# Kernel tuning notes

Measured on AMD Instinct MI355X. Metric: run time of the kernel, lower is better.

Reference implementation:

```python
import jax, jax.numpy as jnp
import numpy as np
from jax import lax

T = 8192; BLK = 32; M = 64; C = 32; D = 512; HH = 256; L = 6; TEMP = 1.0

def _gru(x, Wih, Whh, bih, bhh, reverse=False):
    # x: (S, B, in) -> (S, B, h); PyTorch GRU cell math
    h0 = jnp.zeros((x.shape[1], Whh.shape[0]), x.dtype)
    xs = x[::-1] if reverse else x
    gi = xs @ Wih + bih
    def step(h, g):
        gh = h @ Whh + bhh
        ir, iz, inn = jnp.split(g, 3, -1)
        hr, hz, hn = jnp.split(gh, 3, -1)
        r = jax.nn.sigmoid(ir + hr)
        z = jax.nn.sigmoid(iz + hz)
        n = jnp.tanh(inn + r * hn)
        h = (1.0 - z) * n + z * h
        return h, h
    _, hs = lax.scan(step, h0, gi)
    return hs[::-1] if reverse else hs

def _xattn(X, Y, Xpos, Ypos, Wq, Wk, Wv, Wo, bo):
    # Y queries X; single head with head_dim = D (X2Y_map)
    q = (Y + Ypos) @ Wq
    k = (X + Xpos) @ Wk
    v = X @ Wv
    logits = jnp.einsum('ybd,xbd->byx', q, k) / jnp.sqrt(jnp.float32(q.shape[-1]))
    attn = jax.nn.softmax(logits, -1)
    out = jnp.einsum('byx,xbd->ybd', attn, v) @ Wo + bo
    return out, attn, logits

def _conv1(x, W, b, dil=1):
    y = lax.conv_general_dilated(x, W, (1,), 'SAME', rhs_dilation=(dil,), dimension_numbers=('NCH', 'OIH', 'NCH'))
    return y + b[None, :, None]

def _sim(x, W, b, text):
    v = x @ W + b
    v = v / jnp.linalg.norm(v, axis=-1, keepdims=True)
    t = text / jnp.linalg.norm(text, axis=-1, keepdims=True)
    return jnp.einsum('tbh,ch->tbc', v, t) / TEMP

def _segments(frame_feature, Wf2c, bf2c, text):
    # host-side argmax -> contiguous-run segmentation (mirrors utils.parse_label on CPU)
    sim = _sim(frame_feature, Wf2c, bf2c, text)
    pred = np.asarray(jnp.argmax(sim[:, 0], -1))
    change = np.concatenate([[0], (np.diff(pred) != 0).astype(np.int64)])
    seg_id = np.cumsum(change)
    S = int(seg_id[-1]) + 1
    starts = np.concatenate([[0], np.flatnonzero(change)])
    ends = np.concatenate([starts[1:] - 1, [len(pred) - 1]])
    centers = (starts + ends) // 2
    return jnp.asarray(seg_id), S, jnp.asarray(centers)

def _core(p, seg_id, S, centers):
    ff = p['frame_feature']
    cnt = jax.ops.segment_sum(jnp.ones((T,), jnp.float32), seg_id, S)
    seg = jax.ops.segment_sum(ff, seg_id, S) / cnt[:, None, None]  # frame->seg mean pool
    hf = _gru(seg, p['sg_Wih_f'], p['sg_Whh_f'], p['sg_bih_f'], p['sg_bhh_f'])
    hb = _gru(seg, p['sg_Wih_b'], p['sg_Whh_b'], p['sg_bih_b'], p['sg_bhh_b'], reverse=True)
    seg = jax.nn.relu(jnp.concatenate([hf, hb], -1)) @ p['Wcomb'] + p['bcomb']
    seg_pos = p['frame_pos'][centers]
    af, _, _ = _xattn(seg, p['action_feature'], seg_pos, p['action_pos'], p['f2a_Wq'], p['f2a_Wk'], p['f2a_Wv'], p['f2a_Wo'], p['f2a_bo'])
    af = _gru(af, p['ag_Wih'], p['ag_Whh'], p['ag_bih'], p['ag_bhh'])  # action branch GRU
    seg2, _, _ = _xattn(af, seg, p['action_pos'], seg_pos, p['a2f_Wq'], p['a2f_Wk'], p['a2f_Wv'], p['a2f_Wo'], p['a2f_bo'])
    s2f = seg2[seg_id]  # seg->frame upsample
    ff2 = jax.nn.relu(jnp.concatenate([s2f, ff], -1) @ p['Wsf'] + p['bsf'])
    x = jnp.transpose(ff2[:, 0])[None]  # (1, D, T)
    x = _conv1(x, p['tcn_in_W'], p['tcn_in_b'])
    for i in range(L):  # dilated residual TCN (MSTCN)
        y = jax.nn.relu(_conv1(x, p['tcn_dW'][i], p['tcn_db'][i], dil=2 ** i))
        x = x + _conv1(y, p['tcn_pW'][i], p['tcn_pb'][i])
    x = _conv1(x, p['tcn_out_W'], p['tcn_out_b'])
    ff_out = jnp.transpose(x[0])[:, None, :]
    return ff_out, af, seg2

def setup_inputs():
    ks = iter(jax.random.split(jax.random.key(0), 80))
    def rn(*shape):
        return jax.random.normal(next(ks), shape, dtype=jnp.float32)
    def z(n):
        return jnp.zeros((n,), jnp.float32)
    s = 0.05
    base = rn(T // BLK, 1, D)
    frame_feature = jnp.repeat(base, BLK, axis=0) + 0.01 * rn(T, 1, D)
    return {
        'frame_feature': frame_feature,
        'action_feature': rn(M, 1, D),
        'frame_pos': 0.02 * rn(T, 1, D),
        'action_pos': 0.02 * rn(M, 1, D),
        'text_emb': rn(C, 512),
        'Wf2c': s * rn(D, 512), 'bf2c': z(512),
        'Wa2c': s * rn(D, 512), 'ba2c': z(512),
        'Ws2c': s * rn(D, 512), 'bs2c': z(512),
        'sg_Wih_f': s * rn(D, 3 * HH), 'sg_Whh_f': s * rn(HH, 3 * HH), 'sg_bih_f': z(3 * HH), 'sg_bhh_f': z(3 * HH),
        'sg_Wih_b': s * rn(D, 3 * HH), 'sg_Whh_b': s * rn(HH, 3 * HH), 'sg_bih_b': z(3 * HH), 'sg_bhh_b': z(3 * HH),
        'Wcomb': s * rn(D, D), 'bcomb': z(D),
        'f2a_Wq': s * rn(D, D), 'f2a_Wk': s * rn(D, D), 'f2a_Wv': s * rn(D, D), 'f2a_Wo': s * rn(D, D), 'f2a_bo': z(D),
        'ag_Wih': s * rn(D, 3 * D), 'ag_Whh': s * rn(D, 3 * D), 'ag_bih': z(3 * D), 'ag_bhh': z(3 * D),
        'a2f_Wq': s * rn(D, D), 'a2f_Wk': s * rn(D, D), 'a2f_Wv': s * rn(D, D), 'a2f_Wo': s * rn(D, D), 'a2f_bo': z(D),
        'Wsf': s * rn(2 * D, D), 'bsf': z(D),
        'tcn_in_W': s * rn(D, D, 1), 'tcn_in_b': z(D),
        'tcn_dW': s * rn(L, D, D, 3), 'tcn_db': jnp.zeros((L, D), jnp.float32),
        'tcn_pW': s * rn(L, D, D, 1), 'tcn_pb': jnp.zeros((L, D), jnp.float32),
        'tcn_out_W': s * rn(D, D, 1), 'tcn_out_b': z(D),
    }

def reference(frame_feature, action_feature, frame_pos, action_pos, text_emb, Wf2c, bf2c, Wa2c, ba2c, Ws2c, bs2c, sg_Wih_f, sg_Whh_f, sg_bih_f, sg_bhh_f, sg_Wih_b, sg_Whh_b, sg_bih_b, sg_bhh_b, Wcomb, bcomb, f2a_Wq, f2a_Wk, f2a_Wv, f2a_Wo, f2a_bo, ag_Wih, ag_Whh, ag_bih, ag_bhh, a2f_Wq, a2f_Wk, a2f_Wv, a2f_Wo, a2f_bo, Wsf, bsf, tcn_in_W, tcn_in_b, tcn_dW, tcn_db, tcn_pW, tcn_pb, tcn_out_W, tcn_out_b):
    p = dict(locals())
    seg_id, S, centers = _segments(frame_feature, Wf2c, bf2c, text_emb)
    ff_out, af, seg2 = _core(p, seg_id, S, centers)
    frame_sim = _sim(ff_out, Wf2c, bf2c, text_emb)
    action_sim = _sim(af, Wa2c, ba2c, text_emb)
    seg_sim = _sim(seg2, Ws2c, bs2c, text_emb)
    return ff_out, af, frame_sim, action_sim, seg_sim
```

## Files before the change

### kernel.cpp

```cpp
#include <hip/hip_runtime.h>
#include <cstdint>
#include <cstddef>

__device__ __forceinline__ float sigf(float x) { return 1.f / (1.f + expf(-x)); }

__device__ __forceinline__ unsigned packh(float a, float b) {
  union { unsigned u; _Float16 h[2]; } cv;
  cv.h[0] = (_Float16)a; cv.h[1] = (_Float16)b; return cv.u;
}
__device__ __forceinline__ float2 uph(unsigned u) {
  union { unsigned uu; _Float16 h[2]; } cv; cv.uu = u;
  return make_float2((float)cv.h[0], (float)cv.h[1]);
}

typedef _Float16 f16x8 __attribute__((ext_vector_type(8)));
typedef float f32x16 __attribute__((ext_vector_type(16)));

static constexpr int TT = 8192;
static constexpr int MM = 64;
static constexpr int CC = 32;
static constexpr int DD = 512;
static constexpr unsigned GUARD_MAX = 1u << 30;
static constexpr unsigned HSENT = 0x7FC07FC0u;

__global__ void nanfill_k(float* __restrict__ p, long n) {
  long i = (long)blockIdx.x * 256 + threadIdx.x;
  long stride = (long)gridDim.x * 256;
  const float qnan = __int_as_float(0x7fc00000);
  for (; i < n; i += stride) p[i] = qnan;
}
__global__ void sfill_k(unsigned* __restrict__ p, long n) {
  long i = (long)blockIdx.x * 256 + threadIdx.x;
  long stride = (long)gridDim.x * 256;
  for (; i < n; i += stride) p[i] = HSENT;
}

__global__ void copy_k(const float* __restrict__ a, float* __restrict__ o, int n) {
  int i = blockIdx.x * 256 + threadIdx.x;
  if (i < n) o[i] = a[i];
}
__global__ void addff_k(const float* __restrict__ a, const float* __restrict__ b, float* __restrict__ o, int n) {
  int i = blockIdx.x * 256 + threadIdx.x;
  if (i < n) o[i] = a[i] + b[i];
}
__global__ void acomb_k(const unsigned* __restrict__ hf, const unsigned* __restrict__ hb,
                        float* __restrict__ o, int n) {
  int i = blockIdx.x * 256 + threadIdx.x;
  if (i >= n) return;
  int s = i >> 9, j = i & 511;
  const unsigned pk = (j < 256) ? hf[(size_t)s * 128 + (j >> 1)]
                                : hb[(size_t)s * 128 + ((j - 256) >> 1)];
  const float2 two = uph(pk);
  const float v = (j & 1) ? two.y : two.x;
  o[i] = fmaxf(v, 0.f);
}
__global__ void gatherpos_k(const float* __restrict__ fpos, const int* __restrict__ centers,
                            float* __restrict__ segpos, int n) {
  int i = blockIdx.x * 256 + threadIdx.x;
  if (i >= n) return;
  int s = i >> 9, dd = i & 511;
  int ct = centers[s];
  ct = ct < 0 ? 0 : (ct > TT - 1 ? TT - 1 : ct);
  segpos[i] = fpos[(size_t)ct * 512 + dd];
}

__global__ void tnorm_k(const float* __restrict__ text, float* __restrict__ tnorm) {
  int c = blockIdx.x * 256 + threadIdx.x;
  if (c >= 32) return;
  float s = 0.f;
  for (int dd = 0; dd < 512; dd++) { float v = text[(size_t)c * 512 + dd]; s += v * v; }
  tnorm[c] = sqrtf(s);
}

__global__ void prepM_k(const float* __restrict__ W, const float* __restrict__ b,
                        const float* __restrict__ text, const float* __restrict__ tnorm,
                        float* __restrict__ M, float* __restrict__ bdot) {
  int idx = blockIdx.x * 256 + threadIdx.x;
  if (idx < 512 * 32) {
    int k = idx >> 5, c = idx & 31;
    const float* wr = W + (size_t)k * 512;
    const float* tr = text + (size_t)c * 512;
    float s = 0.f;
    for (int dd = 0; dd < 512; dd++) s += wr[dd] * tr[dd];
    M[idx] = s / tnorm[c];
  }
  if (idx < 32) {
    const float* tr = text + (size_t)idx * 512;
    float s = 0.f;
    for (int dd = 0; dd < 512; dd++) s += b[dd] * tr[dd];
    bdot[idx] = s / tnorm[idx];
  }
}

__launch_bounds__(256)
__global__ void fargmax_k(const float* __restrict__ ff, const float* __restrict__ M,
                          const float* __restrict__ bdot, int* __restrict__ pred) {
  const int r = blockIdx.x * 8 + (threadIdx.x >> 5);
  const int c = threadIdx.x & 31;
  const float* fr = ff + (size_t)r * 512;
  float acc = bdot[c];
  for (int k = 0; k < 512; k++) acc += fr[k] * M[k * 32 + c];
  float best = acc; int bidx = c;
  for (int off = 16; off >= 1; off >>= 1) {
    const float ov = __shfl_xor(best, off);
    const int oi = __shfl_xor(bidx, off);
    if (ov > best || (ov == best && oi < bidx)) { best = ov; bidx = oi; }
  }
  if (c == 0) pred[r] = bidx;
}

__global__ void nlogit_k(const float* __restrict__ Q, const float* __restrict__ Kk,
                         float* __restrict__ L, int NY, int NX) {
  int idx = blockIdx.x * 256 + threadIdx.x;
  if (idx >= NY * NX) return;
  int y = idx / NX, x = idx - y * NX;
  const float* qr = Q + (size_t)y * 512;
  const float* kr = Kk + (size_t)x * 512;
  float d = 0.f;
  for (int k = 0; k < 512; k++) d += qr[k] * kr[k];
  L[idx] = d * 0.044194173824159216f;
}
__global__ void nsoft_k(float* __restrict__ L, int NY, int NX) {
  int y = blockIdx.x * 256 + threadIdx.x;
  if (y >= NY) return;
  float* row = L + (size_t)y * NX;
  float m = row[0];
  for (int x = 1; x < NX; x++) m = fmaxf(m, row[x]);
  float s = 0.f;
  for (int x = 0; x < NX; x++) { float p = expf(row[x] - m); row[x] = p; s += p; }
  const float inv = 1.f / s;
  for (int x = 0; x < NX; x++) row[x] *= inv;
}
__global__ void nav_k(const float* __restrict__ P, const float* __restrict__ V,
                      float* __restrict__ O, int NY, int NX) {
  int idx = blockIdx.x * 256 + threadIdx.x;
  if (idx >= NY * 512) return;
  int y = idx >> 9, dd = idx & 511;
  const float* pr = P + (size_t)y * NX;
  float o = 0.f;
  for (int x = 0; x < NX; x++) o += pr[x] * V[(size_t)x * 512 + dd];
  O[idx] = o;
}

__global__ void segscan_k(const int* __restrict__ pred, int* __restrict__ segid,
                          int* __restrict__ starts, int* __restrict__ centers,
                          int* __restrict__ cnts) {
  __shared__ int base[256];
  __shared__ int SS;
  const int tid = threadIdx.x;
  int lc = 0;
  unsigned flags = 0;
  int prev = (tid > 0) ? pred[tid * 32 - 1] : 0;
  for (int i = 0; i < 32; i++) {
    const int t = tid * 32 + i;
    const int cur = pred[t];
    const int c = (t > 0) && (cur != prev);
    prev = cur;
    flags |= ((unsigned)c) << i;
    lc += c;
  }
  base[tid] = lc;
  __syncthreads();
  if (tid == 0) {
    int run = 0;
    for (int i = 0; i < 256; i++) { const int v = base[i]; base[i] = run; run += v; }
    SS = run + 1;
  }
  __syncthreads();
  int b = base[tid];
  for (int i = 0; i < 32; i++) {
    const int t = tid * 32 + i;
    if ((flags >> i) & 1u) { b++; starts[b] = t; }
    segid[t] = b;
  }
  if (tid == 0) starts[0] = 0;
  __threadfence_block();
  __syncthreads();
  const int S = SS;
  for (int s = tid; s < TT; s += 256) {
    if (s < S) {
      const int e = (s == S - 1) ? (TT - 1) : (starts[s + 1] - 1);
      centers[s] = (starts[s] + e) >> 1;
      cnts[s] = e - starts[s] + 1;
    } else {
      starts[s] = 0; cnts[s] = 1; centers[s] = 0;
    }
  }
}

__global__ void segmean_k(const float* __restrict__ ff, const int* __restrict__ starts,
                          const int* __restrict__ cnts, float* __restrict__ segmean, int S) {
  int idx = blockIdx.x * 256 + threadIdx.x;
  if (idx >= S * 512) return;
  int s = idx >> 9, dd = idx & 511;
  int st = starts[s], n = cnts[s];
  st = st < 0 ? 0 : (st > TT - 1 ? TT - 1 : st);
  n = n < 1 ? 1 : n;
  if (st + n > TT) n = TT - st;
  float a = 0.f;
  for (int t = st; t < st + n; t++) a += ff[(size_t)t * 512 + dd];
  segmean[idx] = a / (float)n;
}

__launch_bounds__(192)
__global__ void gru_seg_mb_k(const float* __restrict__ gi_f, const float* __restrict__ gi_b,
                             const float* __restrict__ Whh_f, const float* __restrict__ bhh_f,
                             const float* __restrict__ Whh_b, const float* __restrict__ bhh_b,
                             unsigned* __restrict__ hf, unsigned* __restrict__ hb, int S) {
  const int dir = blockIdx.x >> 2;
  const int part = blockIdx.x & 3;
  const float* gi = dir ? gi_b : gi_f;
  const float* Whh = dir ? Whh_b : Whh_f;
  const float* bhh = dir ? bhh_b : bhh_f;
  unsigned* ho = dir ? hb : hf;
  const int tid = threadIdx.x;
  const int h0 = part * 64;
  const int w0 = h0 >> 1;
  const int grp = tid >> 6;
  const int jj = tid & 63;
  const int j = grp * 256 + h0 + jj;
  __shared__ __align__(16) unsigned wlds[128 * 192];
  __shared__ __align__(16) unsigned hpk[128];
  __shared__ float rbuf[64], zbuf[64], gnbuf[64];
  for (int e = tid; e < 128 * 192; e += 192) {
    const int q = e / 768, rem = e % 768;
    const int g = rem >> 2, r = rem & 3;
    const int i2 = q * 4 + r;
    const int gg = (g >> 6) * 256 + h0 + (g & 63);
    wlds[e] = packh(Whh[(size_t)(2 * i2) * 768 + gg], Whh[(size_t)(2 * i2 + 1) * 768 + gg]);
  }
  for (int e = tid; e < 128; e += 192) hpk[e] = 0u;
  const float bj = bhh[j];
  float h_reg = 0.f;
  __syncthreads();
  const uint4* hp4 = reinterpret_cast<const uint4*>(hpk);
  const uint4* wp4 = reinterpret_cast<const uint4*>(wlds);
  int s = dir ? (S - 1) : 0;
  float g_j = gi[(size_t)s * 768 + j];
  float g_n = (tid < 64) ? gi[(size_t)s * 768 + 512 + h0 + tid] : 0.f;
  for (int step = 0; step < S; step++) {
    float a0 = 0.f, a1 = 0.f, a2 = 0.f, a3 = 0.f;
#pragma unroll 8
    for (int q = 0; q < 32; q++) {
      const uint4 h4 = hp4[q];
      const uint4 w4 = wp4[q * 192 + tid];
      const float2 hh0 = uph(h4.x), hh1 = uph(h4.y), hh2 = uph(h4.z), hh3 = uph(h4.w);
      const float2 ww0 = uph(w4.x), ww1 = uph(w4.y), ww2 = uph(w4.z), ww3 = uph(w4.w);
      a0 += hh0.x * ww0.x + hh0.y * ww0.y;
      a1 += hh1.x * ww1.x + hh1.y * ww1.y;
      a2 += hh2.x * ww2.x + hh2.y * ww2.y;
      a3 += hh3.x * ww3.x + hh3.y * ww3.y;
    }
    const float gh = bj + (a0 + a1) + (a2 + a3);
    if (grp == 0)      rbuf[jj] = sigf(g_j + gh);
    else if (grp == 1) zbuf[jj] = sigf(g_j + gh);
    else               gnbuf[jj] = gh;
    __syncthreads();
    if (tid < 64) {
      const float nval = tanhf(g_n + rbuf[tid] * gnbuf[tid]);
      const float hn = (1.f - zbuf[tid]) * nval + zbuf[tid] * h_reg;
      h_reg = hn;
      const float hnb = __shfl_down(hn, 1);
      if ((tid & 1) == 0) {
        const unsigned pk = packh(hn, hnb);
        hpk[w0 + (tid >> 1)] = pk;
        __hip_atomic_store(&ho[(size_t)s * 128 + w0 + (tid >> 1)], pk,
                           __ATOMIC_RELAXED, __HIP_MEMORY_SCOPE_AGENT);
      }
    }
    const int sn = dir ? (s - 1) : (s + 1);
    if (step + 1 < S) {
      g_j = gi[(size_t)sn * 768 + j];
      if (tid < 64) g_n = gi[(size_t)sn * 768 + 512 + h0 + tid];
    }
    __syncthreads();
    if (tid < 96) {
      const int re = (tid < w0) ? tid : tid + 32;
      unsigned v = __hip_atomic_load(&ho[(size_t)s * 128 + re],
                                     __ATOMIC_RELAXED, __HIP_MEMORY_SCOPE_AGENT);
      unsigned guard = 0;
      while (v == HSENT && ++guard < GUARD_MAX) {
        __builtin_amdgcn_s_sleep(1);
        v = __hip_atomic_load(&ho[(size_t)s * 128 + re],
                              __ATOMIC_RELAXED, __HIP_MEMORY_SCOPE_AGENT);
      }
      hpk[re] = v;
    }
    __syncthreads();
    s = sn;
  }
}

__launch_bounds__(128)
__global__ void gru_act_mb_k(const float* __restrict__ gi, const float* __restrict__ Whh,
                             const float* __restrict__ bhh, float* __restrict__ hout,
                             int steps) {
  const int part = blockIdx.x;
  const int tid = threadIdx.x;
  const int h0 = part * 32;
  const int grp = tid >> 5;
  const int jj = tid & 31;
  const bool act = (tid < 96);
  const int j = act ? (grp * 512 + h0 + jj) : 0;
  __shared__ __align__(16) unsigned wlds[256 * 96];
  __shared__ __align__(16) unsigned hpk[256];
  __shared__ float rbuf[32], zbuf[32], gnbuf[32];
  for (int e = tid; e < 256 * 96; e += 128) {
    const int q = e / 384, rem = e % 384;
    const int g = rem >> 2, r = rem & 3;
    const int i2 = q * 4 + r;
    const int gg = (g >> 5) * 512 + h0 + (g & 31);
    wlds[e] = packh(Whh[(size_t)(2 * i2) * 1536 + gg], Whh[(size_t)(2 * i2 + 1) * 1536 + gg]);
  }
  for (int e = tid; e < 256; e += 128) hpk[e] = 0u;
  const float bj = act ? bhh[j] : 0.f;
  float h_reg = 0.f;
  __syncthreads();
  const uint4* hp4 = reinterpret_cast<const uint4*>(hpk);
  const uint4* wp4 = reinterpret_cast<const uint4*>(wlds);
  float g_j = act ? gi[j] : 0.f;
  float g_n = (tid < 32) ? gi[1024 + h0 + tid] : 0.f;
  const int gown0 = h0 >> 2;
  for (int step = 0; step < steps; step++) {
    if (act) {
      float a0 = 0.f, a1 = 0.f, a2 = 0.f, a3 = 0.f;
#pragma unroll 8
      for (int q = 0; q < 64; q++) {
        const uint4 h4 = hp4[q];
        const uint4 w4 = wp4[q * 96 + tid];
        const float2 hh0 = uph(h4.x), hh1 = uph(h4.y), hh2 = uph(h4.z), hh3 = uph(h4.w);
        const float2 ww0 = uph(w4.x), ww1 = uph(w4.y), ww2 = uph(w4.z), ww3 = uph(w4.w);
        a0 += hh0.x * ww0.x + hh0.y * ww0.y;
        a1 += hh1.x * ww1.x + hh1.y * ww1.y;
        a2 += hh2.x * ww2.x + hh2.y * ww2.y;
        a3 += hh3.x * ww3.x + hh3.y * ww3.y;
      }
      const float gh = bj + (a0 + a1) + (a2 + a3);
      if (grp == 0)      rbuf[jj] = sigf(g_j + gh);
      else if (grp == 1) zbuf[jj] = sigf(g_j + gh);
      else               gnbuf[jj] = gh;
    }
    __syncthreads();
    if (tid < 32) {
      const float nval = tanhf(g_n + rbuf[tid] * gnbuf[tid]);
      const float hn = (1.f - zbuf[tid]) * nval + zbuf[tid] * h_reg;
      h_reg = hn;
      __hip_atomic_store(&hout[(size_t)step * 512 + h0 + tid], hn,
                         __ATOMIC_RELAXED, __HIP_MEMORY_SCOPE_AGENT);
      const float hnb = __shfl_down(hn, 1);
      if ((tid & 1) == 0) hpk[(h0 + tid) >> 1] = packh(hn, hnb);
    }
    if (step + 1 < steps) {
      if (act) g_j = gi[(size_t)(step + 1) * 1536 + j];
      if (tid < 32) g_n = gi[(size_t)(step + 1) * 1536 + 1024 + h0 + tid];
    }
    __syncthreads();
    {
      const int g = tid;
      if (g < gown0 || g >= gown0 + 8) {
        const float* gp = hout + (size_t)step * 512 + 4 * g;
        float x0, x1, x2, x3;
        unsigned guard = 0;
        do {
          x0 = __hip_atomic_load(gp + 0, __ATOMIC_RELAXED, __HIP_MEMORY_SCOPE_AGENT);
          x1 = __hip_atomic_load(gp + 1, __ATOMIC_RELAXED, __HIP_MEMORY_SCOPE_AGENT);
          x2 = __hip_atomic_load(gp + 2, __ATOMIC_RELAXED, __HIP_MEMORY_SCOPE_AGENT);
          x3 = __hip_atomic_load(gp + 3, __ATOMIC_RELAXED, __HIP_MEMORY_SCOPE_AGENT);
          if (x0 == x0 && x1 == x1 && x2 == x2 && x3 == x3) break;
          __builtin_amdgcn_s_sleep(1);
        } while (++guard < GUARD_MAX);
        hpk[2 * g + 0] = packh(x0, x1);
        hpk[2 * g + 1] = packh(x2, x3);
      }
    }
    __syncthreads();
  }
}

__launch_bounds__(256)
__global__ void gemmm_k(const float* __restrict__ A, const float* __restrict__ B,
                        const float* __restrict__ bias, float* __restrict__ C,
                        int M, int N, int K) {
  __shared__ __align__(16) _Float16 As16[64][72];
  __shared__ __align__(16) _Float16 Bs16[128][72];
  const int n0 = blockIdx.x * 128, m0 = blockIdx.y * 64;
  const int tid = threadIdx.x;
  const int l = tid & 63, w = tid >> 6;
  const int wm = w & 1, wn = w >> 1;
  const int l31 = l & 31, q = l >> 5;
  f32x16 acc0, acc1;
#pragma unroll
  for (int i = 0; i < 16; i++) { acc0[i] = 0.f; acc1[i] = 0.f; }
  const int am = tid >> 2, ak0 = (tid & 3) * 16;
  const int bk = tid >> 2, bn0 = (tid & 3) * 32;
  for (int kc = 0; kc < K; kc += 64) {
    __syncthreads();
#pragma unroll
    for (int kk = 0; kk < 16; kk += 4) {
      const float4 av = *reinterpret_cast<const float4*>(A + (size_t)(m0 + am) * K + kc + ak0 + kk);
      As16[am][ak0 + kk + 0] = (_Float16)av.x; As16[am][ak0 + kk + 1] = (_Float16)av.y;
      As16[am][ak0 + kk + 2] = (_Float16)av.z; As16[am][ak0 + kk + 3] = (_Float16)av.w;
    }
#pragma unroll
    for (int nn = 0; nn < 32; nn += 4) {
      const float4 bv = *reinterpret_cast<const float4*>(B + (size_t)(kc + bk) * N + n0 + bn0 + nn);
      Bs16[bn0 + nn + 0][bk] = (_Float16)bv.x; Bs16[bn0 + nn + 1][bk] = (_Float16)bv.y;
      Bs16[bn0 + nn + 2][bk] = (_Float16)bv.z; Bs16[bn0 + nn + 3][bk] = (_Float16)bv.w;
    }
    __syncthreads();
#pragma unroll
    for (int ks = 0; ks < 4; ks++) {
      const int k0 = ks * 16 + q * 8;
      const f16x8 a = *reinterpret_cast<const f16x8*>(&As16[wm * 32 + l31][k0]);
      const f16x8 b0 = *reinterpret_cast<const f16x8*>(&Bs16[wn * 64 + l31][k0]);
      acc0 = __builtin_amdgcn_mfma_f32_32x32x16_f16(a, b0, acc0, 0, 0, 0);
      const f16x8 b1 = *reinterpret_cast<const f16x8*>(&Bs16[wn * 64 + 32 + l31][k0]);
      acc1 = __builtin_amdgcn_mfma_f32_32x32x16_f16(a, b1, acc1, 0, 0, 0);
    }
  }
#pragma unroll
  for (int r = 0; r < 16; r++) {
    const int m = m0 + wm * 32 + (r & 3) + 8 * (r >> 2) + 4 * q;
    {
      const int n = n0 + wn * 64 + l31;
      float v = acc0[r];
      if (bias) v += bias[n];
      C[(size_t)m * N + n] = v;
    }
    {
      const int n = n0 + wn * 64 + 32 + l31;
      float v = acc1[r];
      if (bias) v += bias[n];
      C[(size_t)m * N + n] = v;
    }
  }
}

__launch_bounds__(256)
__global__ void ff2m_k(const float* __restrict__ seg2, const float* __restrict__ ff,
                       const int* __restrict__ segid, const float* __restrict__ Wsf,
                       const float* __restrict__ bsf, float* __restrict__ Y, int S) {
  __shared__ __align__(16) _Float16 As16[64][72];
  __shared__ __align__(16) _Float16 Bs16[128][72];
  const int t0 = blockIdx.x * 128, nd0 = blockIdx.y * 64;
  const int tid = threadIdx.x;
  const int l = tid & 63, w = tid >> 6;
  const int wm = w & 1, wn = w >> 1;
  const int l31 = l & 31, q = l >> 5;
  f32x16 acc0, acc1;
#pragma unroll
  for (int i = 0; i < 16; i++) { acc0[i] = 0.f; acc1[i] = 0.f; }
  const int ak = tid >> 2, an0 = (tid & 3) * 16;
  const int bt = tid >> 1, bk0 = (tid & 1) * 32;
  const int tglob = t0 + bt;
  int sid = segid[tglob];
  sid = sid < 0 ? 0 : (sid >= S ? S - 1 : sid);
  for (int kc = 0; kc < 1024; kc += 64) {
    __syncthreads();
#pragma unroll
    for (int nn = 0; nn < 16; nn += 4) {
      const float4 wv = *reinterpret_cast<const float4*>(Wsf + (size_t)(kc + ak) * 512 + nd0 + an0 + nn);
      As16[an0 + nn + 0][ak] = (_Float16)wv.x; As16[an0 + nn + 1][ak] = (_Float16)wv.y;
      As16[an0 + nn + 2][ak] = (_Float16)wv.z; As16[an0 + nn + 3][ak] = (_Float16)wv.w;
    }
    {
      const float* src = (kc < 512) ? (seg2 + (size_t)sid * 512 + kc + bk0)
                                    : (ff + (size_t)tglob * 512 + (kc - 512) + bk0);
#pragma unroll
      for (int kk = 0; kk < 32; kk += 4) {
        const float4 xv = *reinterpret_cast<const float4*>(src + kk);
        Bs16[bt][bk0 + kk + 0] = (_Float16)xv.x; Bs16[bt][bk0 + kk + 1] = (_Float16)xv.y;
        Bs16[bt][bk0 + kk + 2] = (_Float16)xv.z; Bs16[bt][bk0 + kk + 3] = (_Float16)xv.w;
      }
    }
    __syncthreads();
#pragma unroll
    for (int ks = 0; ks < 4; ks++) {
      const int k0 = ks * 16 + q * 8;
      const f16x8 a = *reinterpret_cast<const f16x8*>(&As16[wm * 32 + l31][k0]);
      const f16x8 b0 = *reinterpret_cast<const f16x8*>(&Bs16[wn * 64 + l31][k0]);
      acc0 = __builtin_amdgcn_mfma_f32_32x32x16_f16(a, b0, acc0, 0, 0, 0);
      const f16x8 b1 = *reinterpret_cast<const f16x8*>(&Bs16[wn * 64 + 32 + l31][k0]);
      acc1 = __builtin_amdgcn_mfma_f32_32x32x16_f16(a, b1, acc1, 0, 0, 0);
    }
  }
#pragma unroll
  for (int r = 0; r < 16; r++) {
    const int nd = nd0 + wm * 32 + (r & 3) + 8 * (r >> 2) + 4 * q;
    const float bb = bsf[nd];
    {
      const int t = t0 + wn * 64 + l31;
      Y[(size_t)nd * TT + t] = fmaxf(acc0[r] + bb, 0.f);
    }
    {
      const int t = t0 + wn * 64 + 32 + l31;
      Y[(size_t)nd * TT + t] = fmaxf(acc1[r] + bb, 0.f);
    }
  }
}

template<int NTAPS, int RELU, int RES>
__launch_bounds__(256)
__global__ void convm_k(const float* __restrict__ X, const float* __restrict__ W,
                        const float* __restrict__ bias, const float* __restrict__ Res,
                        float* __restrict__ Y, int dil) {
  const int d = (NTAPS == 3) ? dil : 0;
  const int width = 128 + 2 * d;
  __shared__ __align__(16) _Float16 Ws16[NTAPS][64][72];
  __shared__ __align__(16) _Float16 Xs16[192][72];
  const int t0 = blockIdx.x * 128, c0 = blockIdx.y * 64;
  const int tid = threadIdx.x;
  const int l = tid & 63, w = tid >> 6;
  const int wm = w & 1, wn = w >> 1;
  const int l31 = l & 31, q = l >> 5;
  f32x16 acc0, acc1;
#pragma unroll
  for (int i = 0; i < 16; i++) { acc0[i] = 0.f; acc1[i] = 0.f; }
  const int xk = tid >> 2;
  const int xu0 = tid & 3;
  for (int kc = 0; kc < 512; kc += 64) {
    __syncthreads();
    {
      const float* xr = X + (size_t)(kc + xk) * TT;
      for (int u = xu0; u < width; u += 4) {
        const int gt = t0 - d + u;
        const float v = (gt >= 0 && gt < TT) ? xr[gt] : 0.f;
        Xs16[u][xk] = (_Float16)v;
      }
    }
    if (NTAPS == 3) {
      for (int e = tid; e < 64 * 48; e += 256) {
        const int c = e / 48;
        const int f0 = (e - c * 48) * 4;
        const float4 wv = *reinterpret_cast<const float4*>(
            W + (size_t)(c0 + c) * 1536 + (size_t)kc * 3 + f0);
        const float vv[4] = {wv.x, wv.y, wv.z, wv.w};
#pragma unroll
        for (int t = 0; t < 4; t++) {
          const int f = f0 + t;
          Ws16[f % 3][c][f / 3] = (_Float16)vv[t];
        }
      }
    } else {
      for (int e = tid; e < 1024; e += 256) {
        const int c = e >> 4, i0 = (e & 15) << 2;
        const float4 wv = *reinterpret_cast<const float4*>(W + (size_t)(c0 + c) * 512 + kc + i0);
        Ws16[0][c][i0 + 0] = (_Float16)wv.x; Ws16[0][c][i0 + 1] = (_Float16)wv.y;
        Ws16[0][c][i0 + 2] = (_Float16)wv.z; Ws16[0][c][i0 + 3] = (_Float16)wv.w;
      }
    }
    __syncthreads();
#pragma unroll
    for (int tap = 0; tap < NTAPS; tap++) {
#pragma unroll
      for (int ks = 0; ks < 4; ks++) {
        const int k0 = ks * 16 + q * 8;
        const f16x8 a = *reinterpret_cast<const f16x8*>(&Ws16[tap][wm * 32 + l31][k0]);
        const int row0 = wn * 64 + l31 + tap * d;
        const f16x8 b0 = *reinterpret_cast<const f16x8*>(&Xs16[row0][k0]);
        acc0 = __builtin_amdgcn_mfma_f32_32x32x16_f16(a, b0, acc0, 0, 0, 0);
        const f16x8 b1 = *reinterpret_cast<const f16x8*>(&Xs16[row0 + 32][k0]);
        acc1 = __builtin_amdgcn_mfma_f32_32x32x16_f16(a, b1, acc1, 0, 0, 0);
      }
    }
  }
#pragma unroll
  for (int r = 0; r < 16; r++) {
    const int m = wm * 32 + (r & 3) + 8 * (r >> 2) + 4 * q;
    const int c = c0 + m;
    const float bb = bias[c];
    {
      const int t = t0 + wn * 64 + l31;
      float v = acc0[r] + bb;
      if (RES) v += Res[(size_t)c * TT + t];
      if (RELU) v = fmaxf(v, 0.f);
      Y[(size_t)c * TT + t] = v;
    }
    {
      const int t = t0 + wn * 64 + 32 + l31;
      float v = acc1[r] + bb;
      if (RES) v += Res[(size_t)c * TT + t];
      if (RELU) v = fmaxf(v, 0.f);
      Y[(size_t)c * TT + t] = v;
    }
  }
}

__launch_bounds__(256)
__global__ void temit_k(const float* __restrict__ Xin, float* __restrict__ outp,
                        float* __restrict__ Aout) {
  __shared__ float tile[32][33];
  const int t0 = blockIdx.x * 32, d0 = blockIdx.y * 32;
  const int lx = threadIdx.x & 31, ly = threadIdx.x >> 5;
#pragma unroll
  for (int r = 0; r < 4; r++)
    tile[ly + 8 * r][lx] = Xin[(size_t)(d0 + ly + 8 * r) * TT + t0 + lx];
  __syncthreads();
#pragma unroll
  for (int r = 0; r < 4; r++) {
    const int t = t0 + ly + 8 * r, dd = d0 + lx;
    const float v = tile[lx][ly + 8 * r];
    outp[(size_t)t * 512 + dd] = v;
    Aout[(size_t)t * 512 + dd] = v;
  }
}

__launch_bounds__(256)
__global__ void csim_k(const float* __restrict__ V, const float* __restrict__ text,
                       const float* __restrict__ tnorm, float* __restrict__ out) {
  __shared__ float vs[512];
  __shared__ float red[4];
  const int r = blockIdx.x, tid = threadIdx.x;
  const float a = V[(size_t)r * 512 + tid];
  const float b = V[(size_t)r * 512 + 256 + tid];
  vs[tid] = a; vs[tid + 256] = b;
  float ssp = a * a + b * b;
  for (int off = 32; off >= 1; off >>= 1) ssp += __shfl_xor(ssp, off);
  if ((tid & 63) == 0) red[tid >> 6] = ssp;
  __syncthreads();
  const float ss = red[0] + red[1] + red[2] + red[3];
  const int c = tid >> 3, p = tid & 7;
  const float* tr = text + (size_t)c * 512 + p * 64;
  const float* vr = vs + p * 64;
  float d = 0.f;
#pragma unroll
  for (int k = 0; k < 64; k++) d += vr[k] * tr[k];
  for (int off = 4; off >= 1; off >>= 1) d += __shfl_xor(d, off);
  if (p == 0) out[(size_t)r * 32 + c] = d / (sqrtf(ss) * tnorm[c]);
}

extern "C" void kernel_launch(void* const* d_in, const int* in_sizes, int n_in,
                              void* d_out, int out_size, void* d_ws, size_t ws_size,
                              hipStream_t stream) {
  const float* in_ff   = (const float*)d_in[0];
  const float* in_act  = (const float*)d_in[1];
  const float* in_fpos = (const float*)d_in[2];
  const float* in_apos = (const float*)d_in[3];
  const float* in_text = (const float*)d_in[4];
  const float* Wf2c = (const float*)d_in[5];  const float* bf2c = (const float*)d_in[6];
  const float* Wa2c = (const float*)d_in[7];  const float* ba2c = (const float*)d_in[8];
  const float* Ws2c = (const float*)d_in[9];  const float* bs2c = (const float*)d_in[10];
  const float* Wih_f = (const float*)d_in[11]; const float* Whh_f = (const float*)d_in[12];
  const float* bih_f = (const float*)d_in[13]; const float* bhh_f = (const float*)d_in[14];
  const float* Wih_b = (const float*)d_in[15]; const float* Whh_b = (const float*)d_in[16];
  const float* bih_b = (const float*)d_in[17]; const float* bhh_b = (const float*)d_in[18];
  const float* Wcomb = (const float*)d_in[19]; const float* bcomb = (const float*)d_in[20];
  const float* f2a_Wq = (const float*)d_in[21]; const float* f2a_Wk = (const float*)d_in[22];
  const float* f2a_Wv = (const float*)d_in[23]; const float* f2a_Wo = (const float*)d_in[24];
  const float* f2a_bo = (const float*)d_in[25];
  const float* ag_Wih = (const float*)d_in[26]; const float* ag_Whh = (const float*)d_in[27];
  const float* ag_bih = (const float*)d_in[28]; const float* ag_bhh = (const float*)d_in[29];
  const float* a2f_Wq = (const float*)d_in[30]; const float* a2f_Wk = (const float*)d_in[31];
  const float* a2f_Wv = (const float*)d_in[32]; const float* a2f_Wo = (const float*)d_in[33];
  const float* a2f_bo = (const float*)d_in[34];
  const float* Wsf = (const float*)d_in[35]; const float* bsf = (const float*)d_in[36];
  const float* tcn_inW = (const float*)d_in[37]; const float* tcn_inb = (const float*)d_in[38];
  const float* tcn_dW = (const float*)d_in[39]; const float* tcn_db = (const float*)d_in[40];
  const float* tcn_pW = (const float*)d_in[41]; const float* tcn_pb = (const float*)d_in[42];
  const float* tcn_outW = (const float*)d_in[43]; const float* tcn_outb = (const float*)d_in[44];

  int S = (out_size - (TT * DD + MM * DD + TT * CC + MM * CC)) / CC;
  if (S < 1) S = 1;
  if (S > TT) S = TT;
  const int Spad = (S + 63) & ~63;

  char* ws = (char*)d_ws;
  size_t off = 0;
  auto alloc = [&](size_t b) -> char* { char* p = ws + off; off += (b + 255) & ~(size_t)255; return p; };
  float* Mmat = (float*)alloc((size_t)512 * 32 * 4);
  float* bdot = (float*)alloc(32 * 4);
  const size_t BTD = (size_t)TT * DD * 4;
  float* bufA = (float*)alloc(BTD);
  float* bufB = (float*)alloc(BTD);
  int* pred    = (int*)alloc((size_t)TT * 4);
  int* segid   = (int*)alloc((size_t)TT * 4);
  int* starts  = (int*)alloc((size_t)TT * 4);
  int* centers = (int*)alloc((size_t)TT * 4);
  int* cnts    = (int*)alloc((size_t)TT * 4);
  float* tnorm = (float*)alloc(32 * 4);
  float* segmean = (float*)alloc((size_t)Spad * 512 * 4);
  float* gif  = (float*)alloc((size_t)Spad * 768 * 4);
  float* gib  = (float*)alloc((size_t)Spad * 768 * 4);
  unsigned* hfb = (unsigned*)alloc((size_t)Spad * 128 * 4);
  unsigned* hbb = (unsigned*)alloc((size_t)Spad * 128 * 4);
  float* acmb = (float*)alloc((size_t)Spad * 512 * 4);
  float* segc = (float*)alloc((size_t)Spad * 512 * 4);
  float* segpos = (float*)alloc((size_t)Spad * 512 * 4);
  float* kin  = (float*)alloc((size_t)Spad * 512 * 4);
  float* kf2a = (float*)alloc((size_t)Spad * 512 * 4);
  float* vf2a = (float*)alloc((size_t)Spad * 512 * 4);
  float* q2   = (float*)alloc((size_t)Spad * 512 * 4);
  float* att2 = (float*)alloc((size_t)Spad * 512 * 4);
  float* seg2 = (float*)alloc((size_t)Spad * 512 * 4);
  float* vseg = (float*)alloc((size_t)Spad * 512 * 4);
  float* pbuf = (float*)alloc((size_t)64 * Spad * 4);
  float* qin  = (float*)alloc((size_t)64 * 512 * 4);
  float* qf2a = (float*)alloc((size_t)64 * 512 * 4);
  float* att1 = (float*)alloc((size_t)64 * 512 * 4);
  float* af0  = (float*)alloc((size_t)64 * 512 * 4);
  float* aggi = (float*)alloc((size_t)64 * 1536 * 4);
  float* afg  = (float*)alloc((size_t)64 * 512 * 4);
  float* k2in = (float*)alloc((size_t)64 * 512 * 4);
  float* k2   = (float*)alloc((size_t)64 * 512 * 4);
  float* v2   = (float*)alloc((size_t)64 * 512 * 4);
  float* vaf  = (float*)alloc((size_t)64 * 512 * 4);
  (void)ws_size; (void)in_sizes; (void)n_in;

  float* outp = (float*)d_out;
  float* out_ff   = outp;
  float* out_af   = outp + (size_t)TT * DD;
  float* out_fsim = out_af + (size_t)MM * DD;
  float* out_asim = out_fsim + (size_t)TT * CC;
  float* out_ssim = out_asim + (size_t)MM * CC;

  auto GR = [](long n) { return (unsigned)((n + 255) / 256); };
  const unsigned Sg = (unsigned)(Spad / 64);

  tnorm_k<<<1, 256, 0, stream>>>(in_text, tnorm);

  sfill_k<<<64, 256, 0, stream>>>(hfb, (long)Spad * 128);
  sfill_k<<<64, 256, 0, stream>>>(hbb, (long)Spad * 128);
  nanfill_k<<<32, 256, 0, stream>>>(afg, (long)64 * 512);

  prepM_k<<<64, 256, 0, stream>>>(Wf2c, bf2c, in_text, tnorm, Mmat, bdot);
  fargmax_k<<<TT / 8, 256, 0, stream>>>(in_ff, Mmat, bdot, pred);
  segscan_k<<<1, 256, 0, stream>>>(pred, segid, starts, centers, cnts);
  segmean_k<<<GR((long)S * 512), 256, 0, stream>>>(in_ff, starts, cnts, segmean, S);

  gemmm_k<<<dim3(6, Sg), 256, 0, stream>>>(segmean, Wih_f, bih_f, gif, Spad, 768, 512);
  gemmm_k<<<dim3(6, Sg), 256, 0, stream>>>(segmean, Wih_b, bih_b, gib, Spad, 768, 512);
  gru_seg_mb_k<<<8, 192, 0, stream>>>(gif, gib, Whh_f, bhh_f, Whh_b, bhh_b, hfb, hbb, S);
  acomb_k<<<GR((long)S * 512), 256, 0, stream>>>(hfb, hbb, acmb, S * 512);
  gemmm_k<<<dim3(4, Sg), 256, 0, stream>>>(acmb, Wcomb, bcomb, segc, Spad, 512, 512);
  gatherpos_k<<<GR((long)S * 512), 256, 0, stream>>>(in_fpos, centers, segpos, S * 512);

  addff_k<<<GR(64 * 512), 256, 0, stream>>>(in_act, in_apos, qin, 64 * 512);
  addff_k<<<GR((long)S * 512), 256, 0, stream>>>(segc, segpos, kin, S * 512);
  gemmm_k<<<dim3(4, 1), 256, 0, stream>>>(qin, f2a_Wq, nullptr, qf2a, 64, 512, 512);
  gemmm_k<<<dim3(4, Sg), 256, 0, stream>>>(kin, f2a_Wk, nullptr, kf2a, Spad, 512, 512);
  gemmm_k<<<dim3(4, Sg), 256, 0, stream>>>(segc, f2a_Wv, nullptr, vf2a, Spad, 512, 512);
  nlogit_k<<<GR((long)64 * S), 256, 0, stream>>>(qf2a, kf2a, pbuf, 64, S);
  nsoft_k<<<1, 256, 0, stream>>>(pbuf, 64, S);
  nav_k<<<GR(64 * 512), 256, 0, stream>>>(pbuf, vf2a, att1, 64, S);
  gemmm_k<<<dim3(4, 1), 256, 0, stream>>>(att1, f2a_Wo, f2a_bo, af0, 64, 512, 512);

  gemmm_k<<<dim3(12, 1), 256, 0, stream>>>(af0, ag_Wih, ag_bih, aggi, 64, 1536, 512);
  gru_act_mb_k<<<16, 128, 0, stream>>>(aggi, ag_Whh, ag_bhh, afg, MM);
  copy_k<<<GR(64 * 512), 256, 0, stream>>>(afg, out_af, 64 * 512);

  addff_k<<<GR(64 * 512), 256, 0, stream>>>(afg, in_apos, k2in, 64 * 512);
  gemmm_k<<<dim3(4, Sg), 256, 0, stream>>>(kin, a2f_Wq, nullptr, q2, Spad, 512, 512);
  gemmm_k<<<dim3(4, 1), 256, 0, stream>>>(k2in, a2f_Wk, nullptr, k2, 64, 512, 512);
  gemmm_k<<<dim3(4, 1), 256, 0, stream>>>(afg, a2f_Wv, nullptr, v2, 64, 512, 512);
  nlogit_k<<<GR((long)S * 64), 256, 0, stream>>>(q2, k2, pbuf, S, 64);
  nsoft_k<<<GR(S), 256, 0, stream>>>(pbuf, S, 64);
  nav_k<<<GR((long)S * 512), 256, 0, stream>>>(pbuf, v2, att2, S, 64);
  gemmm_k<<<dim3(4, Sg), 256, 0, stream>>>(att2, a2f_Wo, a2f_bo, seg2, Spad, 512, 512);

  ff2m_k<<<dim3(64, 8), 256, 0, stream>>>(seg2, in_ff, segid, Wsf, bsf, bufA, S);
  convm_k<1, 0, 0><<<dim3(64, 8), 256, 0, stream>>>(bufA, tcn_inW, tcn_inb, nullptr, bufB, 1);
  for (int l = 0; l < 6; l++) {
    convm_k<3, 1, 0><<<dim3(64, 8), 256, 0, stream>>>(
        bufB, tcn_dW + (size_t)l * 512 * 512 * 3, tcn_db + (size_t)l * 512, nullptr, bufA, 1 << l);
    convm_k<1, 0, 1><<<dim3(64, 8), 256, 0, stream>>>(
        bufA, tcn_pW + (size_t)l * 512 * 512, tcn_pb + (size_t)l * 512, bufB, bufB, 1);
  }
  convm_k<1, 0, 0><<<dim3(64, 8), 256, 0, stream>>>(bufB, tcn_outW, tcn_outb, nullptr, bufA, 1);
  temit_k<<<dim3(256, 16), 256, 0, stream>>>(bufA, out_ff, bufB);

  gemmm_k<<<dim3(4, 128), 256, 0, stream>>>(bufB, Wf2c, bf2c, bufA, TT, 512, 512);
  csim_k<<<TT, 256, 0, stream>>>(bufA, in_text, tnorm, out_fsim);
  gemmm_k<<<dim3(4, 1), 256, 0, stream>>>(afg, Wa2c, ba2c, vaf, 64, 512, 512);
  csim_k<<<64, 256, 0, stream>>>(vaf, in_text, tnorm, out_asim);
  gemmm_k<<<dim3(4, Sg), 256, 0, stream>>>(seg2, Ws2c, bs2c, vseg, Spad, 512, 512);
  csim_k<<<(unsigned)S, 256, 0, stream>>>(vseg, in_text, tnorm, out_ssim);
}
```

Measured before the change: 3.761 ms.

## Move cross-attention logits and AV products to MFMA GEMMs, fuse position adds

The naive per-element logit, softmax and attention-value kernels are replaced by an MFMA-based Q·K^T kernel, a block-parallel row softmax that zero-fills padded columns, and the existing MFMA GEMM for P·V. The separate elementwise add kernels for positional embeddings are folded into the GEMM A-operand load through an optional second input. This removes scalar dot-product loops and several launches and intermediate buffers. In exchange, the logits and probabilities now pass through fp16 in the MFMA path, and correctness relies on padded rows and columns being handled by the zero-fill and the Mv guard.

```diff
diff --git a/kernel.cpp b/kernel.cpp
--- a/kernel.cpp
+++ b/kernel.cpp
@@ -38,10 +38,6 @@
 __global__ void copy_k(const float* __restrict__ a, float* __restrict__ o, int n) {
   int i = blockIdx.x * 256 + threadIdx.x;
   if (i < n) o[i] = a[i];
-}
-__global__ void addff_k(const float* __restrict__ a, const float* __restrict__ b, float* __restrict__ o, int n) {
-  int i = blockIdx.x * 256 + threadIdx.x;
-  if (i < n) o[i] = a[i] + b[i];
 }
 __global__ void acomb_k(const unsigned* __restrict__ hf, const unsigned* __restrict__ hb,
                         float* __restrict__ o, int n) {
@@ -107,39 +103,6 @@
     if (ov > best || (ov == best && oi < bidx)) { best = ov; bidx = oi; }
   }
   if (c == 0) pred[r] = bidx;
-}
-
-__global__ void nlogit_k(const float* __restrict__ Q, const float* __restrict__ Kk,
-                         float* __restrict__ L, int NY, int NX) {
-  int idx = blockIdx.x * 256 + threadIdx.x;
-  if (idx >= NY * NX) return;
-  int y = idx / NX, x = idx - y * NX;
-  const float* qr = Q + (size_t)y * 512;
-  const float* kr = Kk + (size_t)x * 512;
-  float d = 0.f;
-  for (int k = 0; k < 512; k++) d += qr[k] * kr[k];
-  L[idx] = d * 0.044194173824159216f;
-}
-__global__ void nsoft_k(float* __restrict__ L, int NY, int NX) {
-  int y = blockIdx.x * 256 + threadIdx.x;
-  if (y >= NY) return;
-  float* row = L + (size_t)y * NX;
-  float m = row[0];
-  for (int x = 1; x < NX; x++) m = fmaxf(m, row[x]);
-  float s = 0.f;
-  for (int x = 0; x < NX; x++) { float p = expf(row[x] - m); row[x] = p; s += p; }
-  const float inv = 1.f / s;
-  for (int x = 0; x < NX; x++) row[x] *= inv;
-}
-__global__ void nav_k(const float* __restrict__ P, const float* __restrict__ V,
-                      float* __restrict__ O, int NY, int NX) {
-  int idx = blockIdx.x * 256 + threadIdx.x;
-  if (idx >= NY * 512) return;
-  int y = idx >> 9, dd = idx & 511;
-  const float* pr = P + (size_t)y * NX;
-  float o = 0.f;
-  for (int x = 0; x < NX; x++) o += pr[x] * V[(size_t)x * 512 + dd];
-  O[idx] = o;
 }
 
 __global__ void segscan_k(const int* __restrict__ pred, int* __restrict__ segid,
@@ -378,7 +341,8 @@
 }
 
 __launch_bounds__(256)
-__global__ void gemmm_k(const float* __restrict__ A, const float* __restrict__ B,
+__global__ void gemmm_k(const float* __restrict__ A, const float* __restrict__ A2,
+                        const float* __restrict__ B,
                         const float* __restrict__ bias, float* __restrict__ C,
                         int M, int N, int K) {
   __shared__ __align__(16) _Float16 As16[64][72];
@@ -397,7 +361,11 @@
     __syncthreads();
 #pragma unroll
     for (int kk = 0; kk < 16; kk += 4) {
-      const float4 av = *reinterpret_cast<const float4*>(A + (size_t)(m0 + am) * K + kc + ak0 + kk);
+      float4 av = *reinterpret_cast<const float4*>(A + (size_t)(m0 + am) * K + kc + ak0 + kk);
+      if (A2) {
+        const float4 a2 = *reinterpret_cast<const float4*>(A2 + (size_t)(m0 + am) * K + kc + ak0 + kk);
+        av.x += a2.x; av.y += a2.y; av.z += a2.z; av.w += a2.w;
+      }
       As16[am][ak0 + kk + 0] = (_Float16)av.x; As16[am][ak0 + kk + 1] = (_Float16)av.y;
       As16[am][ak0 + kk + 2] = (_Float16)av.z; As16[am][ak0 + kk + 3] = (_Float16)av.w;
     }
@@ -434,6 +402,74 @@
       C[(size_t)m * N + n] = v;
     }
   }
+}
+
+__launch_bounds__(256)
+__global__ void gemmnt_k(const float* __restrict__ A, const float* __restrict__ B,
+                         float* __restrict__ C, int Mv, int Nld, int K, float scale) {
+  __shared__ __align__(16) _Float16 As16[64][72];
+  __shared__ __align__(16) _Float16 Bs16[64][72];
+  const int n0 = blockIdx.x * 64, m0 = blockIdx.y * 64;
+  const int tid = threadIdx.x;
+  const int l = tid & 63, w = tid >> 6;
+  const int wm = w & 1, wn = w >> 1;
+  const int l31 = l & 31, q = l >> 5;
+  f32x16 acc;
+#pragma unroll
+  for (int i = 0; i < 16; i++) acc[i] = 0.f;
+  const int am = tid >> 2, ak0 = (tid & 3) * 16;
+  for (int kc = 0; kc < K; kc += 64) {
+    __syncthreads();
+#pragma unroll
+    for (int kk = 0; kk < 16; kk += 4) {
+      const float4 av = *reinterpret_cast<const float4*>(A + (size_t)(m0 + am) * K + kc + ak0 + kk);
+      As16[am][ak0 + kk + 0] = (_Float16)av.x; As16[am][ak0 + kk + 1] = (_Float16)av.y;
+      As16[am][ak0 + kk + 2] = (_Float16)av.z; As16[am][ak0 + kk + 3] = (_Float16)av.w;
+      const float4 bv = *reinterpret_cast<const float4*>(B + (size_t)(n0 + am) * K + kc + ak0 + kk);
+      Bs16[am][ak0 + kk + 0] = (_Float16)bv.x; Bs16[am][ak0 + kk + 1] = (_Float16)bv.y;
+      Bs16[am][ak0 + kk + 2] = (_Float16)bv.z; Bs16[am][ak0 + kk + 3] = (_Float16)bv.w;
+    }
+    __syncthreads();
+#pragma unroll
+    for (int ks = 0; ks < 4; ks++) {
+      const int k0 = ks * 16 + q * 8;
+      const f16x8 a = *reinterpret_cast<const f16x8*>(&As16[wm * 32 + l31][k0]);
+      const f16x8 b = *reinterpret_cast<const f16x8*>(&Bs16[wn * 32 + l31][k0]);
+      acc = __builtin_amdgcn_mfma_f32_32x32x16_f16(a, b, acc, 0, 0, 0);
+    }
+  }
+#pragma unroll
+  for (int r = 0; r < 16; r++) {
+    const int m = m0 + wm * 32 + (r & 3) + 8 * (r >> 2) + 4 * q;
+    const int n = n0 + wn * 32 + l31;
+    if (m < Mv) C[(size_t)m * Nld + n] = acc[r] * scale;
+  }
+}
+
+__launch_bounds__(256)
+__global__ void psoft_k(float* __restrict__ L, int NXs, int NV) {
+  float* row = L + (size_t)blockIdx.x * NXs;
+  __shared__ float redm[4], reds[4];
+  const int tid = threadIdx.x;
+  float m = -3.4e38f;
+  for (int x = tid; x < NV; x += 256) m = fmaxf(m, row[x]);
+  for (int off = 32; off >= 1; off >>= 1) m = fmaxf(m, __shfl_xor(m, off));
+  if ((tid & 63) == 0) redm[tid >> 6] = m;
+  __syncthreads();
+  m = fmaxf(fmaxf(redm[0], redm[1]), fmaxf(redm[2], redm[3]));
+  float s = 0.f;
+  for (int x = tid; x < NV; x += 256) {
+    const float p = expf(row[x] - m);
+    row[x] = p;
+    s += p;
+  }
+  for (int off = 32; off >= 1; off >>= 1) s += __shfl_xor(s, off);
+  if ((tid & 63) == 0) reds[tid >> 6] = s;
+  __syncthreads();
+  s = reds[0] + reds[1] + reds[2] + reds[3];
+  const float inv = 1.f / s;
+  for (int x = tid; x < NV; x += 256) row[x] *= inv;
+  for (int x = NV + tid; x < NXs; x += 256) row[x] = 0.f;
 }
 
 __launch_bounds__(256)
@@ -686,7 +722,6 @@
   float* acmb = (float*)alloc((size_t)Spad * 512 * 4);
   float* segc = (float*)alloc((size_t)Spad * 512 * 4);
   float* segpos = (float*)alloc((size_t)Spad * 512 * 4);
-  float* kin  = (float*)alloc((size_t)Spad * 512 * 4);
   float* kf2a = (float*)alloc((size_t)Spad * 512 * 4);
   float* vf2a = (float*)alloc((size_t)Spad * 512 * 4);
   float* q2   = (float*)alloc((size_t)Spad * 512 * 4);
@@ -694,13 +729,11 @@
   float* seg2 = (float*)alloc((size_t)Spad * 512 * 4);
   float* vseg = (float*)alloc((size_t)Spad * 512 * 4);
   float* pbuf = (float*)alloc((size_t)64 * Spad * 4);
-  float* qin  = (float*)alloc((size_t)64 * 512 * 4);
   float* qf2a = (float*)alloc((size_t)64 * 512 * 4);
   float* att1 = (float*)alloc((size_t)64 * 512 * 4);
   float* af0  = (float*)alloc((size_t)64 * 512 * 4);
   float* aggi = (float*)alloc((size_t)64 * 1536 * 4);
   float* afg  = (float*)alloc((size_t)64 * 512 * 4);
-  float* k2in = (float*)alloc((size_t)64 * 512 * 4);
   float* k2   = (float*)alloc((size_t)64 * 512 * 4);
   float* v2   = (float*)alloc((size_t)64 * 512 * 4);
   float* vaf  = (float*)alloc((size_t)64 * 512 * 4);
@@ -715,6 +748,7 @@
 
   auto GR = [](long n) { return (unsigned)((n + 255) / 256); };
   const unsigned Sg = (unsigned)(Spad / 64);
+  const float ATTS = 0.044194173824159216f;
 
   tnorm_k<<<1, 256, 0, stream>>>(in_text, tnorm);
 
@@ -727,35 +761,32 @@
   segscan_k<<<1, 256, 0, stream>>>(pred, segid, starts, centers, cnts);
   segmean_k<<<GR((long)S * 512), 256, 0, stream>>>(in_ff, starts, cnts, segmean, S);
 
-  gemmm_k<<<dim3(6, Sg), 256, 0, stream>>>(segmean, Wih_f, bih_f, gif, Spad, 768, 512);
-  gemmm_k<<<dim3(6, Sg), 256, 0, stream>>>(segmean, Wih_b, bih_b, gib, Spad, 768, 512);
+  gemmm_k<<<dim3(6, Sg), 256, 0, stream>>>(segmean, nullptr, Wih_f, bih_f, gif, Spad, 768, 512);
+  gemmm_k<<<dim3(6, Sg), 256, 0, stream>>>(segmean, nullptr, Wih_b, bih_b, gib, Spad, 768, 512);
   gru_seg_mb_k<<<8, 192, 0, stream>>>(gif, gib, Whh_f, bhh_f, Whh_b, bhh_b, hfb, hbb, S);
   acomb_k<<<GR((long)S * 512), 256, 0, stream>>>(hfb, hbb, acmb, S * 512);
-  gemmm_k<<<dim3(4, Sg), 256, 0, stream>>>(acmb, Wcomb, bcomb, segc, Spad, 512, 512);
+  gemmm_k<<<dim3(4, Sg), 256, 0, stream>>>(acmb, nullptr, Wcomb, bcomb, segc, Spad, 512, 512);
   gatherpos_k<<<GR((long)S * 512), 256, 0, stream>>>(in_fpos, centers, segpos, S * 512);
 
-  addff_k<<<GR(64 * 512), 256, 0, stream>>>(in_act, in_apos, qin, 64 * 512);
-  addff_k<<<GR((long)S * 512), 256, 0, stream>>>(segc, segpos, kin, S * 512);
-  gemmm_k<<<dim3(4, 1), 256, 0, stream>>>(qin, f2a_Wq, nullptr, qf2a, 64, 512, 512);
-  gemmm_k<<<dim3(4, Sg), 256, 0, stream>>>(kin, f2a_Wk, nullptr, kf2a, Spad, 512, 512);
-  gemmm_k<<<dim3(4, Sg), 256, 0, stream>>>(segc, f2a_Wv, nullptr, vf2a, Spad, 512, 512);
-  nlogit_k<<<GR((long)64 * S), 256, 0, stream>>>(qf2a, kf2a, pbuf, 64, S);
-  nsoft_k<<<1, 256, 0, stream>>>(pbuf, 64, S);
-  nav_k<<<GR(64 * 512), 256, 0, stream>>>(pbuf, vf2a, att1, 64, S);
-  gemmm_k<<<dim3(4, 1), 256, 0, stream>>>(att1, f2a_Wo, f2a_bo, af0, 64, 512, 512);
-
-  gemmm_k<<<dim3(12, 1), 256, 0, stream>>>(af0, ag_Wih, ag_bih, aggi, 64, 1536, 512);
+  gemmm_k<<<dim3(4, 1), 256, 0, stream>>>(in_act, in_apos, f2a_Wq, nullptr, qf2a, 64, 512, 512);
+  gemmm_k<<<dim3(4, Sg), 256, 0, stream>>>(segc, segpos, f2a_Wk, nullptr, kf2a, Spad, 512, 512);
+  gemmm_k<<<dim3(4, Sg), 256, 0, stream>>>(segc, nullptr, f2a_Wv, nullptr, vf2a, Spad, 512, 512);
+  gemmnt_k<<<dim3(Spad / 64, 1), 256, 0, stream>>>(qf2a, kf2a, pbuf, 64, Spad, 512, ATTS);
+  psoft_k<<<64, 256, 0, stream>>>(pbuf, Spad, S);
+  gemmm_k<<<dim3(4, 1), 256, 0, stream>>>(pbuf, nullptr, vf2a, nullptr, att1, 64, 512, Spad);
+  gemmm_k<<<dim3(4, 1), 256, 0, stream>>>(att1, nullptr, f2a_Wo, f2a_bo, af0, 64, 512, 512);
+
+  gemmm_k<<<dim3(12, 1), 256, 0, stream>>>(af0, nullptr, ag_Wih, ag_bih, aggi, 64, 1536, 512);
   gru_act_mb_k<<<16, 128, 0, stream>>>(aggi, ag_Whh, ag_bhh, afg, MM);
   copy_k<<<GR(64 * 512), 256, 0, stream>>>(afg, out_af, 64 * 512);
 
-  addff_k<<<GR(64 * 512), 256, 0, stream>>>(afg, in_apos, k2in, 64 * 512);
-  gemmm_k<<<dim3(4, Sg), 256, 0, stream>>>(kin, a2f_Wq, nullptr, q2, Spad, 512, 512);
-  gemmm_k<<<dim3(4, 1), 256, 0, stream>>>(k2in, a2f_Wk, nullptr, k2, 64, 512, 512);
-  gemmm_k<<<dim3(4, 1), 256, 0, stream>>>(afg, a2f_Wv, nullptr, v2, 64, 512, 512);
-  nlogit_k<<<GR((long)S * 64), 256, 0, stream>>>(q2, k2, pbuf, S, 64);
-  nsoft_k<<<GR(S), 256, 0, stream>>>(pbuf, S, 64);
-  nav_k<<<GR((long)S * 512), 256, 0, stream>>>(pbuf, v2, att2, S, 64);
-  gemmm_k<<<dim3(4, Sg), 256, 0, stream>>>(att2, a2f_Wo, a2f_bo, seg2, Spad, 512, 512);
+  gemmm_k<<<dim3(4, Sg), 256, 0, stream>>>(segc, segpos, a2f_Wq, nullptr, q2, Spad, 512, 512);
+  gemmm_k<<<dim3(4, 1), 256, 0, stream>>>(afg, in_apos, a2f_Wk, nullptr, k2, 64, 512, 512);
+  gemmm_k<<<dim3(4, 1), 256, 0, stream>>>(afg, nullptr, a2f_Wv, nullptr, v2, 64, 512, 512);
+  gemmnt_k<<<dim3(1, Spad / 64), 256, 0, stream>>>(q2, k2, pbuf, S, 64, 512, ATTS);
+  psoft_k<<<(unsigned)S, 256, 0, stream>>>(pbuf, 64, 64);
+  gemmm_k<<<dim3(4, Sg), 256, 0, stream>>>(pbuf, nullptr, v2, nullptr, att2, Spad, 512, 64);
+  gemmm_k<<<dim3(4, Sg), 256, 0, stream>>>(att2, nullptr, a2f_Wo, a2f_bo, seg2, Spad, 512, 512);
 
   ff2m_k<<<dim3(64, 8), 256, 0, stream>>>(seg2, in_ff, segid, Wsf, bsf, bufA, S);
   convm_k<1, 0, 0><<<dim3(64, 8), 256, 0, stream>>>(bufA, tcn_inW, tcn_inb, nullptr, bufB, 1);
@@ -768,10 +799,10 @@
   convm_k<1, 0, 0><<<dim3(64, 8), 256, 0, stream>>>(bufB, tcn_outW, tcn_outb, nullptr, bufA, 1);
   temit_k<<<dim3(256, 16), 256, 0, stream>>>(bufA, out_ff, bufB);
 
-  gemmm_k<<<dim3(4, 128), 256, 0, stream>>>(bufB, Wf2c, bf2c, bufA, TT, 512, 512);
+  gemmm_k<<<dim3(4, 128), 256, 0, stream>>>(bufB, nullptr, Wf2c, bf2c, bufA, TT, 512, 512);
   csim_k<<<TT, 256, 0, stream>>>(bufA, in_text, tnorm, out_fsim);
-  gemmm_k<<<dim3(4, 1), 256, 0, stream>>>(afg, Wa2c, ba2c, vaf, 64, 512, 512);
+  gemmm_k<<<dim3(4, 1), 256, 0, stream>>>(afg, nullptr, Wa2c, ba2c, vaf, 64, 512, 512);
   csim_k<<<64, 256, 0, stream>>>(vaf, in_text, tnorm, out_asim);
-  gemmm_k<<<dim3(4, Sg), 256, 0, stream>>>(seg2, Ws2c, bs2c, vseg, Spad, 512, 512);
+  gemmm_k<<<dim3(4, Sg), 256, 0, stream>>>(seg2, nullptr, Ws2c, bs2c, vseg, Spad, 512, 512);
   csim_k<<<(unsigned)S, 256, 0, stream>>>(vseg, in_text, tnorm, out_ssim);
 }
```

Measured after the change: 3.417 ms. 1.1x faster.
